# Kernel optimization log

Hardware: AMD Instinct MI355X
Metric: run time of the kernel (lower is better)

## Reference

```python
import jax, jax.numpy as jnp
import numpy as np

D_MODEL = 512
N_HEAD = 8
D_FF = 2048
HEAD = D_MODEL // N_HEAD
B, S = 2, 4096
LN_EPS = 1e-5


def _layernorm(x, g, b):
    mu = jnp.mean(x, axis=-1, keepdims=True)
    var = jnp.mean(jnp.square(x - mu), axis=-1, keepdims=True)
    return (x - mu) * jax.lax.rsqrt(var + LN_EPS) * g + b


def setup_inputs() -> dict:
    key = jax.random.key(0)
    ks = jax.random.split(key, 12)
    s = 0.02
    inp = {
        "src": jax.random.normal(ks[0], (B, S, D_MODEL), dtype=jnp.float32),
        "mask": jnp.ones((B, S, S), dtype=jnp.float32),
        "Wq": jax.random.normal(ks[1], (D_MODEL, D_MODEL), dtype=jnp.float32) * s,
        "bq": jnp.zeros((D_MODEL,), dtype=jnp.float32),
        "Wk": jax.random.normal(ks[2], (D_MODEL, D_MODEL), dtype=jnp.float32) * s,
        "bk": jnp.zeros((D_MODEL,), dtype=jnp.float32),
        "Wv": jax.random.normal(ks[3], (D_MODEL, D_MODEL), dtype=jnp.float32) * s,
        "bv": jnp.zeros((D_MODEL,), dtype=jnp.float32),
        "Wo": jax.random.normal(ks[4], (D_MODEL, D_MODEL), dtype=jnp.float32) * s,
        "bo": jnp.zeros((D_MODEL,), dtype=jnp.float32),
        "W1": jax.random.normal(ks[5], (D_FF, D_MODEL), dtype=jnp.float32) * s,
        "b1": jnp.zeros((D_FF,), dtype=jnp.float32),
        "W2": jax.random.normal(ks[6], (D_MODEL, D_FF), dtype=jnp.float32) * s,
        "b2": jnp.zeros((D_MODEL,), dtype=jnp.float32),
        "ln1_g": jnp.ones((D_MODEL,), dtype=jnp.float32),
        "ln1_b": jnp.zeros((D_MODEL,), dtype=jnp.float32),
        "ln2_g": jnp.ones((D_MODEL,), dtype=jnp.float32),
        "ln2_b": jnp.zeros((D_MODEL,), dtype=jnp.float32),
    }
    return inp


def reference(src, mask, Wq, bq, Wk, bk, Wv, bv, Wo, bo, W1, b1, W2, b2,
              ln1_g, ln1_b, ln2_g, ln2_b):
    # --- multi-head self-attention (chunk/cat == head split on last dim) ---
    def heads(x, W, b):
        y = x @ W.T + b  # [B,S,D]
        return y.reshape(B, S, N_HEAD, HEAD)
    Q = heads(src, Wq, bq)
    K = heads(src, Wk, bk)
    V = heads(src, Wv, bv)
    score = jnp.einsum('bihd,bjhd->bhij', Q, K) / jnp.sqrt(jnp.float32(HEAD))
    score = score + ((1.0 - mask) * -1e9)[:, None, :, :]
    attn = jax.nn.softmax(score, axis=-1)
    ctx = jnp.einsum('bhij,bjhd->bihd', attn, V).reshape(B, S, D_MODEL)
    sa = ctx @ Wo.T + bo
    # --- residual + LN1 ---
    x = _layernorm(src + sa, ln1_g, ln1_b)
    # --- FFN (relu) + residual + LN2 ---
    ff = jax.nn.relu(x @ W1.T + b1) @ W2.T + b2
    return _layernorm(x + ff, ln2_g, ln2_b)
```

## Files before the change

### kernel.cpp

```cpp
#include <hip/hip_runtime.h>
#include <cstdint>
#include <cstddef>

#define DM   512
#define SQL  4096
#define NHE  8
#define HDM  64
#define DFF  2048
#define NB   2

typedef unsigned short u16t;
typedef __attribute__((ext_vector_type(8))) __bf16 bf16x8;
typedef __attribute__((ext_vector_type(4))) float f32x4;
typedef __attribute__((ext_vector_type(8))) unsigned short us8;
typedef __attribute__((ext_vector_type(4))) unsigned short us4;
typedef __attribute__((ext_vector_type(4))) short s16x4;

__device__ inline f32x4 mfma16(bf16x8 a, bf16x8 b, f32x4 c) {
    return __builtin_amdgcn_mfma_f32_16x16x32_bf16(a, b, c, 0, 0, 0);
}
__device__ inline f32x4 mfma16k16(s16x4 a, s16x4 b, f32x4 c) {
    return __builtin_amdgcn_mfma_f32_16x16x16bf16_1k(a, b, c, 0, 0, 0);
}

__device__ inline void load_lds16(const void* g, void* l) {
    __builtin_amdgcn_global_load_lds(
        (const __attribute__((address_space(1))) unsigned int*)g,
        (__attribute__((address_space(3))) unsigned int*)l, 16, 0, 0);
}

__device__ inline u16t f2bf(float x) {
    union { float f; unsigned int u; } v; v.f = x;
    unsigned int r = v.u + 0x7fffu + ((v.u >> 16) & 1u);
    return (u16t)(r >> 16);
}

__device__ inline void store_out(float* C, size_t idx, float v) { C[idx] = v; }
__device__ inline void store_out(u16t* C, size_t idx, float v) { C[idx] = f2bf(v); }

__global__ __launch_bounds__(256) void convert_all(
    const float* __restrict__ src, const float* __restrict__ Wq,
    const float* __restrict__ Wk, const float* __restrict__ Wv,
    const float* __restrict__ Wo, const float* __restrict__ W1,
    const float* __restrict__ W2, const float* __restrict__ bq,
    const float* __restrict__ bk, const float* __restrict__ bv,
    u16t* __restrict__ srcbf, u16t* __restrict__ wqkv, u16t* __restrict__ woc,
    u16t* __restrict__ w1c, u16t* __restrict__ w2c,
    float* __restrict__ bqkv, int* __restrict__ flag) {
    const int blk = blockIdx.x;
    const float* s;
    u16t* d;
    int base;
    if (blk < 2048)      { s = src; d = srcbf;           base = blk; }
    else if (blk < 2176) { s = Wq;  d = wqkv;            base = blk - 2048; }
    else if (blk < 2304) { s = Wk;  d = wqkv + 262144;   base = blk - 2176; }
    else if (blk < 2432) { s = Wv;  d = wqkv + 524288;   base = blk - 2304; }
    else if (blk < 2560) { s = Wo;  d = woc;             base = blk - 2432; }
    else if (blk < 3072) { s = W1;  d = w1c;             base = blk - 2560; }
    else if (blk < 3584) { s = W2;  d = w2c;             base = blk - 3072; }
    else {
        for (int i = threadIdx.x; i < 1536; i += 256)
            bqkv[i] = (i < 512) ? bq[i] : (i < 1024 ? bk[i - 512] : bv[i - 1024]);
        if (threadIdx.x == 0) flag[0] = 1;
        return;
    }
    const int i = base * 2048 + threadIdx.x * 8;
    f32x4 a = *(const f32x4*)(s + i);
    f32x4 b = *(const f32x4*)(s + i + 4);
    us8 o;
    o[0] = f2bf(a[0]); o[1] = f2bf(a[1]); o[2] = f2bf(a[2]); o[3] = f2bf(a[3]);
    o[4] = f2bf(b[0]); o[5] = f2bf(b[1]); o[6] = f2bf(b[2]); o[7] = f2bf(b[3]);
    *(us8*)(d + i) = o;
}

__global__ __launch_bounds__(256) void check_mask_k(const f32x4* __restrict__ m, int* flag) {
    const size_t n4 = (size_t)NB * SQL * SQL / 4;
    size_t i = (size_t)blockIdx.x * 256 + threadIdx.x;
    bool bad = false;
    for (; i < n4; i += (size_t)gridDim.x * 256) {
        f32x4 v = m[i];
        bad |= (v[0] != 1.0f) || (v[1] != 1.0f) || (v[2] != 1.0f) || (v[3] != 1.0f);
    }
    if (bad) flag[0] = 0;
}

template <typename OutT, bool RELU>
__global__ __launch_bounds__(256, 3) void gemm_bt(const u16t* __restrict__ A,
                                                  const u16t* __restrict__ Bw,
                                                  const float* __restrict__ bias,
                                                  OutT* __restrict__ C,
                                                  const int M, const int N, const int K,
                                                  const int ldc) {
    __shared__ u16t As[128 * 32];
    __shared__ u16t Bs[128 * 32];
    const int tid = threadIdx.x;
    const int w = tid >> 6, lane = tid & 63;
    const int l15 = lane & 15, quad = lane >> 4;
    const int m0 = blockIdx.y * 128, n0 = blockIdx.x * 128;
    const int wm = w >> 1, wn = w & 1;

    f32x4 acc[4][4] = {};

    const u16t* Ag = A + ((size_t)(m0 + w * 32 + (lane >> 2))) * K + (lane & 3) * 8;
    const u16t* Bg = Bw + ((size_t)(n0 + w * 32 + (lane >> 2))) * K + (lane & 3) * 8;
    u16t* Asw = &As[(w * 32) * 32];
    u16t* Bsw = &Bs[(w * 32) * 32];

    for (int k0 = 0; k0 < K; k0 += 32) {
        __syncthreads();
        load_lds16(Ag + k0, Asw);
        load_lds16(Ag + (size_t)16 * K + k0, Asw + 16 * 32);
        load_lds16(Bg + k0, Bsw);
        load_lds16(Bg + (size_t)16 * K + k0, Bsw + 16 * 32);
        __syncthreads();
        bf16x8 af[4], bfr[4];
#pragma unroll
        for (int mt = 0; mt < 4; ++mt)
            af[mt] = *(const bf16x8*)&As[(wm * 64 + mt * 16 + l15) * 32 + quad * 8];
#pragma unroll
        for (int nt = 0; nt < 4; ++nt)
            bfr[nt] = *(const bf16x8*)&Bs[(wn * 64 + nt * 16 + l15) * 32 + quad * 8];
#pragma unroll
        for (int mt = 0; mt < 4; ++mt)
#pragma unroll
            for (int nt = 0; nt < 4; ++nt)
                acc[mt][nt] = mfma16(af[mt], bfr[nt], acc[mt][nt]);
    }

    float bv[4];
#pragma unroll
    for (int nt = 0; nt < 4; ++nt) bv[nt] = bias[n0 + wn * 64 + nt * 16 + l15];
#pragma unroll
    for (int mt = 0; mt < 4; ++mt)
#pragma unroll
        for (int r = 0; r < 4; ++r) {
            const int row = m0 + wm * 64 + mt * 16 + quad * 4 + r;
#pragma unroll
            for (int nt = 0; nt < 4; ++nt) {
                float v = acc[mt][nt][r] + bv[nt];
                if (RELU) v = fmaxf(v, 0.0f);
                store_out(C, (size_t)row * ldc + n0 + wn * 64 + nt * 16 + l15, v);
            }
        }
}

__global__ __launch_bounds__(256) void transpose_v(const u16t* __restrict__ qkv,
                                                   u16t* __restrict__ vt) {
    __shared__ u16t t[64 * 72];
    const int sb = blockIdx.x, h = blockIdx.y, b = blockIdx.z;
    const int tid = threadIdx.x;
#pragma unroll
    for (int it = 0; it < 2; ++it) {
        const int idx = it * 256 + tid;
        const int r = idx >> 3, c8 = idx & 7;
        const u16t* gp = qkv + (size_t)(b * SQL + sb * 64 + r) * (3 * DM) + 2 * DM + h * HDM + c8 * 8;
        *(us8*)&t[r * 72 + c8 * 8] = *(const us8*)gp;
    }
    __syncthreads();
#pragma unroll
    for (int it = 0; it < 2; ++it) {
        const int idx = it * 256 + tid;
        const int d = idx >> 3, s8 = idx & 7;
        us8 o;
#pragma unroll
        for (int u = 0; u < 8; ++u) o[u] = t[(s8 * 8 + u) * 72 + d];
        u16t* gp = vt + (size_t)((b * NHE + h) * HDM + d) * SQL + sb * 64 + s8 * 8;
        *(us8*)gp = o;
    }
}

__global__ __launch_bounds__(256, 2) void flash_attn(const u16t* __restrict__ qkv,
                                                     const u16t* __restrict__ vtg,
                                                     const float* __restrict__ mask,
                                                     const int* __restrict__ flag,
                                                     u16t* __restrict__ ctx) {
    __shared__ u16t Ks[128 * 64];
    __shared__ u16t Vs[64 * 128];

    const int qt = blockIdx.x, h = blockIdx.y, b = blockIdx.z;
    const int tid = threadIdx.x;
    const int w = tid >> 6, lane = tid & 63;
    const int l15 = lane & 15, quad = lane >> 4;
    const int e3 = l15 & 7;
    const bool allones = (*flag != 0);

    bf16x8 qf[2][2];
#pragma unroll
    for (int mt = 0; mt < 2; ++mt) {
        const size_t rowb = (size_t)(b * SQL + qt * 128 + w * 32 + mt * 16 + l15) * (3 * DM) + h * HDM;
#pragma unroll
        for (int kk = 0; kk < 2; ++kk)
            qf[mt][kk] = *(const bf16x8*)(qkv + rowb + kk * 32 + quad * 8);
    }

    f32x4 oacc[4][2] = {};
    float m_r[2] = {-3.0e38f, -3.0e38f};
    float l_r[2] = {0.0f, 0.0f};

    const int r8 = lane >> 3, c8 = lane & 7;
    const int r4 = lane >> 4, c16 = lane & 15;

    for (int kt = 0; kt < SQL / 128; ++kt) {
        const int j0 = kt * 128;
        __syncthreads();
#pragma unroll
        for (int i = 0; i < 4; ++i) {
            const int row = j0 + w * 32 + i * 8 + r8;
            load_lds16(qkv + (size_t)(b * SQL + row) * (3 * DM) + DM + h * HDM + ((c8 ^ r8) * 8),
                       &Ks[(w * 32 + i * 8) * 64]);
        }
#pragma unroll
        for (int i = 0; i < 4; ++i) {
            const int d = w * 16 + i * 4 + r4;
            load_lds16(vtg + (size_t)((b * NHE + h) * HDM + d) * SQL + j0 + ((c16 ^ ((i * 4 + r4) & 7)) * 8),
                       &Vs[(w * 16 + i * 4) * 128]);
        }
        __syncthreads();

        f32x4 sacc[2][8] = {};
#pragma unroll
        for (int kk = 0; kk < 2; ++kk) {
#pragma unroll
            for (int jt = 0; jt < 8; ++jt) {
                bf16x8 af = *(const bf16x8*)&Ks[(jt * 16 + l15) * 64 + (((kk * 4 + quad) ^ e3) * 8)];
                sacc[0][jt] = mfma16(af, qf[0][kk], sacc[0][jt]);
                sacc[1][jt] = mfma16(af, qf[1][kk], sacc[1][jt]);
            }
        }

        float av[2][4];
#pragma unroll
        for (int mt = 0; mt < 2; ++mt) {
            if (!allones) {
                const int gi = qt * 128 + w * 32 + mt * 16 + l15;
#pragma unroll
                for (int jt = 0; jt < 8; ++jt)
#pragma unroll
                    for (int r = 0; r < 4; ++r) {
                        const int gj = j0 + jt * 16 + quad * 4 + r;
                        sacc[mt][jt][r] = sacc[mt][jt][r] * 0.125f
                                        + (1.0f - mask[((size_t)b * SQL + gi) * SQL + gj]) * (-1.0e9f);
                    }
            }
            float mx = -3.0e38f;
#pragma unroll
            for (int jt = 0; jt < 8; ++jt)
#pragma unroll
                for (int r = 0; r < 4; ++r) mx = fmaxf(mx, sacc[mt][jt][r]);
            mx = fmaxf(mx, __shfl_xor(mx, 16));
            mx = fmaxf(mx, __shfl_xor(mx, 32));
            const float cs = allones ? 0.18033688011112042f : 1.4426950408889634f;
            const float mnew = fmaxf(m_r[mt], mx);
            const float mb = mnew * cs;
            const float alpha = exp2f(fmaf(m_r[mt], cs, -mb));
            m_r[mt] = mnew;
            float rsum = 0.0f;
#pragma unroll
            for (int jt = 0; jt < 8; ++jt)
#pragma unroll
                for (int r = 0; r < 4; ++r) {
                    const float p = exp2f(fmaf(sacc[mt][jt][r], cs, -mb));
                    sacc[mt][jt][r] = p;
                    rsum += p;
                }
            rsum += __shfl_xor(rsum, 16);
            rsum += __shfl_xor(rsum, 32);
            l_r[mt] = l_r[mt] * alpha + rsum;
#pragma unroll
            for (int r = 0; r < 4; ++r) av[mt][r] = __shfl(alpha, quad * 4 + r);
#pragma unroll
            for (int dt = 0; dt < 4; ++dt)
#pragma unroll
                for (int r = 0; r < 4; ++r) oacc[dt][mt][r] *= av[mt][r];
        }

#pragma unroll
        for (int jt = 0; jt < 8; ++jt) {
            s16x4 pa0, pa1;
#pragma unroll
            for (int r = 0; r < 4; ++r) {
                pa0[r] = (short)f2bf(sacc[0][jt][r]);
                pa1[r] = (short)f2bf(sacc[1][jt][r]);
            }
            const int vcol = (((2 * jt + (quad >> 1)) ^ e3) * 8) + (quad & 1) * 4;
#pragma unroll
            for (int dt = 0; dt < 4; ++dt) {
                s16x4 vb = *(const s16x4*)&Vs[(dt * 16 + l15) * 128 + vcol];
                oacc[dt][0] = mfma16k16(pa0, vb, oacc[dt][0]);
                oacc[dt][1] = mfma16k16(pa1, vb, oacc[dt][1]);
            }
        }
    }

#pragma unroll
    for (int mt = 0; mt < 2; ++mt) {
        float lv[4];
#pragma unroll
        for (int r = 0; r < 4; ++r) lv[r] = __shfl(l_r[mt], quad * 4 + r);
#pragma unroll
        for (int r = 0; r < 4; ++r) {
            const float inv = 1.0f / lv[r];
            const int token = qt * 128 + w * 32 + mt * 16 + quad * 4 + r;
            const size_t base = (size_t)(b * SQL + token) * DM + h * HDM;
#pragma unroll
            for (int dt = 0; dt < 4; ++dt)
                ctx[base + dt * 16 + l15] = f2bf(oacc[dt][mt][r] * inv);
        }
    }
}

template <bool WBF>
__global__ __launch_bounds__(256) void ln_fused(const float* __restrict__ xa,
                                                const float* __restrict__ xb,
                                                const float* __restrict__ g,
                                                const float* __restrict__ be,
                                                float* __restrict__ outf,
                                                u16t* __restrict__ outh) {
    const int row = blockIdx.x * 4 + (threadIdx.x >> 6);
    const int lane = threadIdx.x & 63;
    const size_t base = (size_t)row * DM;
    f32x4 a0 = *(const f32x4*)(xa + base + lane * 4);
    f32x4 b0 = *(const f32x4*)(xb + base + lane * 4);
    f32x4 a1 = *(const f32x4*)(xa + base + 256 + lane * 4);
    f32x4 b1 = *(const f32x4*)(xb + base + 256 + lane * 4);
    f32x4 v0 = a0 + b0, v1 = a1 + b1;
    float s = v0[0] + v0[1] + v0[2] + v0[3] + v1[0] + v1[1] + v1[2] + v1[3];
    float q = v0[0]*v0[0] + v0[1]*v0[1] + v0[2]*v0[2] + v0[3]*v0[3]
            + v1[0]*v1[0] + v1[1]*v1[1] + v1[2]*v1[2] + v1[3]*v1[3];
#pragma unroll
    for (int off = 1; off < 64; off <<= 1) {
        s += __shfl_xor(s, off);
        q += __shfl_xor(q, off);
    }
    const float mean = s * (1.0f / DM);
    const float var = q * (1.0f / DM) - mean * mean;
    const float rs = rsqrtf(var + 1e-5f);
    f32x4 g0 = *(const f32x4*)(g + lane * 4);
    f32x4 g1 = *(const f32x4*)(g + 256 + lane * 4);
    f32x4 e0 = *(const f32x4*)(be + lane * 4);
    f32x4 e1 = *(const f32x4*)(be + 256 + lane * 4);
    f32x4 y0, y1;
#pragma unroll
    for (int i = 0; i < 4; ++i) {
        y0[i] = (v0[i] - mean) * rs * g0[i] + e0[i];
        y1[i] = (v1[i] - mean) * rs * g1[i] + e1[i];
    }
    *(f32x4*)(outf + base + lane * 4) = y0;
    *(f32x4*)(outf + base + 256 + lane * 4) = y1;
    if (WBF) {
        us4 h0, h1;
#pragma unroll
        for (int i = 0; i < 4; ++i) { h0[i] = f2bf(y0[i]); h1[i] = f2bf(y1[i]); }
        *(us4*)(outh + base + lane * 4) = h0;
        *(us4*)(outh + base + 256 + lane * 4) = h1;
    }
}

extern "C" void kernel_launch(void* const* d_in, const int* in_sizes, int n_in,
                              void* d_out, int out_size, void* d_ws, size_t ws_size,
                              hipStream_t stream) {
    const float* src  = (const float*)d_in[0];
    const float* mask = (const float*)d_in[1];
    const float* Wq = (const float*)d_in[2];
    const float* bq = (const float*)d_in[3];
    const float* Wk = (const float*)d_in[4];
    const float* bk = (const float*)d_in[5];
    const float* Wv = (const float*)d_in[6];
    const float* bv = (const float*)d_in[7];
    const float* Wo = (const float*)d_in[8];
    const float* bo = (const float*)d_in[9];
    const float* W1 = (const float*)d_in[10];
    const float* b1 = (const float*)d_in[11];
    const float* W2 = (const float*)d_in[12];
    const float* b2 = (const float*)d_in[13];
    const float* ln1g = (const float*)d_in[14];
    const float* ln1b = (const float*)d_in[15];
    const float* ln2g = (const float*)d_in[16];
    const float* ln2b = (const float*)d_in[17];

    const int M = NB * SQL;

    char* p = (char*)d_ws;
    auto take = [&](size_t bytes) {
        char* r = p;
        p += (bytes + 1023) & ~(size_t)1023;
        return r;
    };
    u16t* regA   = (u16t*)take((size_t)M * DFF * 2);
    u16t* vtb    = (u16t*)take((size_t)NB * NHE * HDM * SQL * 2);
    u16t* ctxb   = (u16t*)take((size_t)M * DM * 2);
    float* sa_ff = (float*)take((size_t)M * DM * 4);
    float* x1f   = (float*)take((size_t)M * DM * 4);
    u16t* x1h    = (u16t*)take((size_t)M * DM * 2);
    u16t* srcbf  = (u16t*)take((size_t)M * DM * 2);
    u16t* wqkv   = (u16t*)take((size_t)3 * DM * DM * 2);
    float* bqkv  = (float*)take((size_t)3 * DM * 4);
    u16t* woc    = (u16t*)take((size_t)DM * DM * 2);
    u16t* w1c    = (u16t*)take((size_t)DFF * DM * 2);
    u16t* w2c    = (u16t*)take((size_t)DM * DFF * 2);
    int* flag    = (int*)take(1024);
    u16t* qkvb   = regA;
    u16t* hbuf   = regA;

    convert_all<<<3585, 256, 0, stream>>>(src, Wq, Wk, Wv, Wo, W1, W2, bq, bk, bv,
                                          srcbf, wqkv, woc, w1c, w2c, bqkv, flag);
    check_mask_k<<<4096, 256, 0, stream>>>((const f32x4*)mask, flag);

    gemm_bt<u16t, false><<<dim3(12, 64), 256, 0, stream>>>(srcbf, wqkv, bqkv, qkvb,
                                                           M, 3 * DM, DM, 3 * DM);
    transpose_v<<<dim3(SQL / 64, NHE, NB), 256, 0, stream>>>(qkvb, vtb);
    flash_attn<<<dim3(SQL / 128, NHE, NB), 256, 0, stream>>>(qkvb, vtb, mask, flag, ctxb);
    gemm_bt<float, false><<<dim3(4, 64), 256, 0, stream>>>(ctxb, woc, bo, sa_ff,
                                                           M, DM, DM, DM);
    ln_fused<true><<<M / 4, 256, 0, stream>>>(src, sa_ff, ln1g, ln1b, x1f, x1h);
    gemm_bt<u16t, true><<<dim3(16, 64), 256, 0, stream>>>(x1h, w1c, b1, hbuf,
                                                          M, DFF, DM, DFF);
    gemm_bt<float, false><<<dim3(4, 64), 256, 0, stream>>>(hbuf, w2c, b2, sa_ff,
                                                           M, DM, DFF, DM);
    ln_fused<false><<<M / 4, 256, 0, stream>>>(x1f, sa_ff, ln2g, ln2b, (float*)d_out,
                                               (u16t*)nullptr);
}
```

Before: 518.1 us.

## Fold mask check into convert kernel, add native exp2, packed bf16, narrower GEMM tiles

Moves the all-ones mask scan into the conversion kernel as extra blocks, which removes one launch. The flag now defaults to not-bad and is set to a sentinel when a non-one entry is found. Flash attention switches to the native exp2 intrinsic and packs probability pairs into bf16 with a perm instruction that rounds half-up instead of to nearest-even. The GEMM gets a templated N tile, and the two N=512 GEMMs use 64-wide tiles so they launch twice as many blocks and fill more CUs.

```diff
diff --git a/kernel.cpp b/kernel.cpp
--- a/kernel.cpp
+++ b/kernel.cpp
@@ -16,6 +16,9 @@
 typedef __attribute__((ext_vector_type(4))) unsigned short us4;
 typedef __attribute__((ext_vector_type(4))) short s16x4;
 
+extern "C" __device__ float __ocml_native_exp2_f32(float);
+__device__ inline float ex2(float x) { return __ocml_native_exp2_f32(x); }
+
 __device__ inline f32x4 mfma16(bf16x8 a, bf16x8 b, f32x4 c) {
     return __builtin_amdgcn_mfma_f32_16x16x32_bf16(a, b, c, 0, 0, 0);
 }
@@ -33,6 +36,12 @@
     union { float f; unsigned int u; } v; v.f = x;
     unsigned int r = v.u + 0x7fffu + ((v.u >> 16) & 1u);
     return (u16t)(r >> 16);
+}
+
+__device__ inline unsigned int pk_bf2(float lo, float hi) {
+    union { float f; unsigned int u; } a, b;
+    a.f = lo; b.f = hi;
+    return __builtin_amdgcn_perm(b.u + 0x8000u, a.u + 0x8000u, 0x07060302u);
 }
 
 __device__ inline void store_out(float* C, size_t idx, float v) { C[idx] = v; }
@@ -44,6 +53,7 @@
     const float* __restrict__ Wo, const float* __restrict__ W1,
     const float* __restrict__ W2, const float* __restrict__ bq,
     const float* __restrict__ bk, const float* __restrict__ bv,
+    const f32x4* __restrict__ mask4,
     u16t* __restrict__ srcbf, u16t* __restrict__ wqkv, u16t* __restrict__ woc,
     u16t* __restrict__ w1c, u16t* __restrict__ w2c,
     float* __restrict__ bqkv, int* __restrict__ flag) {
@@ -58,10 +68,19 @@
     else if (blk < 2560) { s = Wo;  d = woc;             base = blk - 2432; }
     else if (blk < 3072) { s = W1;  d = w1c;             base = blk - 2560; }
     else if (blk < 3584) { s = W2;  d = w2c;             base = blk - 3072; }
-    else {
+    else if (blk == 3584) {
         for (int i = threadIdx.x; i < 1536; i += 256)
             bqkv[i] = (i < 512) ? bq[i] : (i < 1024 ? bk[i - 512] : bv[i - 1024]);
-        if (threadIdx.x == 0) flag[0] = 1;
+        return;
+    } else {
+        const size_t n4 = (size_t)NB * SQL * SQL / 4;
+        size_t i = (size_t)(blk - 3585) * 256 + threadIdx.x;
+        bool bad = false;
+        for (; i < n4; i += (size_t)2048 * 256) {
+            f32x4 v = mask4[i];
+            bad |= (v[0] != 1.0f) || (v[1] != 1.0f) || (v[2] != 1.0f) || (v[3] != 1.0f);
+        }
+        if (bad) flag[0] = 42;
         return;
     }
     const int i = base * 2048 + threadIdx.x * 8;
@@ -73,18 +92,7 @@
     *(us8*)(d + i) = o;
 }
 
-__global__ __launch_bounds__(256) void check_mask_k(const f32x4* __restrict__ m, int* flag) {
-    const size_t n4 = (size_t)NB * SQL * SQL / 4;
-    size_t i = (size_t)blockIdx.x * 256 + threadIdx.x;
-    bool bad = false;
-    for (; i < n4; i += (size_t)gridDim.x * 256) {
-        f32x4 v = m[i];
-        bad |= (v[0] != 1.0f) || (v[1] != 1.0f) || (v[2] != 1.0f) || (v[3] != 1.0f);
-    }
-    if (bad) flag[0] = 0;
-}
-
-template <typename OutT, bool RELU>
+template <typename OutT, bool RELU, int BN>
 __global__ __launch_bounds__(256, 3) void gemm_bt(const u16t* __restrict__ A,
                                                   const u16t* __restrict__ Bw,
                                                   const float* __restrict__ bias,
@@ -92,54 +100,56 @@
                                                   const int M, const int N, const int K,
                                                   const int ldc) {
     __shared__ u16t As[128 * 32];
-    __shared__ u16t Bs[128 * 32];
+    __shared__ u16t Bs[BN * 32];
+    constexpr int NT = BN / 32;
     const int tid = threadIdx.x;
     const int w = tid >> 6, lane = tid & 63;
     const int l15 = lane & 15, quad = lane >> 4;
-    const int m0 = blockIdx.y * 128, n0 = blockIdx.x * 128;
+    const int m0 = blockIdx.y * 128, n0 = blockIdx.x * BN;
     const int wm = w >> 1, wn = w & 1;
 
-    f32x4 acc[4][4] = {};
+    f32x4 acc[4][NT] = {};
 
     const u16t* Ag = A + ((size_t)(m0 + w * 32 + (lane >> 2))) * K + (lane & 3) * 8;
-    const u16t* Bg = Bw + ((size_t)(n0 + w * 32 + (lane >> 2))) * K + (lane & 3) * 8;
+    const u16t* Bg = Bw + ((size_t)(n0 + w * (BN / 4) + (lane >> 2))) * K + (lane & 3) * 8;
     u16t* Asw = &As[(w * 32) * 32];
-    u16t* Bsw = &Bs[(w * 32) * 32];
+    u16t* Bsw = &Bs[(w * (BN / 4)) * 32];
 
     for (int k0 = 0; k0 < K; k0 += 32) {
         __syncthreads();
         load_lds16(Ag + k0, Asw);
         load_lds16(Ag + (size_t)16 * K + k0, Asw + 16 * 32);
-        load_lds16(Bg + k0, Bsw);
-        load_lds16(Bg + (size_t)16 * K + k0, Bsw + 16 * 32);
+#pragma unroll
+        for (int i = 0; i < BN / 64; ++i)
+            load_lds16(Bg + (size_t)(16 * i) * K + k0, Bsw + i * 16 * 32);
         __syncthreads();
-        bf16x8 af[4], bfr[4];
+        bf16x8 af[4], bfr[NT];
 #pragma unroll
         for (int mt = 0; mt < 4; ++mt)
             af[mt] = *(const bf16x8*)&As[(wm * 64 + mt * 16 + l15) * 32 + quad * 8];
 #pragma unroll
-        for (int nt = 0; nt < 4; ++nt)
-            bfr[nt] = *(const bf16x8*)&Bs[(wn * 64 + nt * 16 + l15) * 32 + quad * 8];
+        for (int nt = 0; nt < NT; ++nt)
+            bfr[nt] = *(const bf16x8*)&Bs[(wn * (BN / 2) + nt * 16 + l15) * 32 + quad * 8];
 #pragma unroll
         for (int mt = 0; mt < 4; ++mt)
 #pragma unroll
-            for (int nt = 0; nt < 4; ++nt)
+            for (int nt = 0; nt < NT; ++nt)
                 acc[mt][nt] = mfma16(af[mt], bfr[nt], acc[mt][nt]);
     }
 
-    float bv[4];
-#pragma unroll
-    for (int nt = 0; nt < 4; ++nt) bv[nt] = bias[n0 + wn * 64 + nt * 16 + l15];
+    float bv[NT];
+#pragma unroll
+    for (int nt = 0; nt < NT; ++nt) bv[nt] = bias[n0 + wn * (BN / 2) + nt * 16 + l15];
 #pragma unroll
     for (int mt = 0; mt < 4; ++mt)
 #pragma unroll
         for (int r = 0; r < 4; ++r) {
             const int row = m0 + wm * 64 + mt * 16 + quad * 4 + r;
 #pragma unroll
-            for (int nt = 0; nt < 4; ++nt) {
+            for (int nt = 0; nt < NT; ++nt) {
                 float v = acc[mt][nt][r] + bv[nt];
                 if (RELU) v = fmaxf(v, 0.0f);
-                store_out(C, (size_t)row * ldc + n0 + wn * 64 + nt * 16 + l15, v);
+                store_out(C, (size_t)row * ldc + n0 + wn * (BN / 2) + nt * 16 + l15, v);
             }
         }
 }
@@ -182,7 +192,7 @@
     const int w = tid >> 6, lane = tid & 63;
     const int l15 = lane & 15, quad = lane >> 4;
     const int e3 = l15 & 7;
-    const bool allones = (*flag != 0);
+    const bool allones = (*flag != 42);
 
     bf16x8 qf[2][2];
 #pragma unroll
@@ -252,14 +262,14 @@
             const float cs = allones ? 0.18033688011112042f : 1.4426950408889634f;
             const float mnew = fmaxf(m_r[mt], mx);
             const float mb = mnew * cs;
-            const float alpha = exp2f(fmaf(m_r[mt], cs, -mb));
+            const float alpha = ex2(fmaf(m_r[mt], cs, -mb));
             m_r[mt] = mnew;
             float rsum = 0.0f;
 #pragma unroll
             for (int jt = 0; jt < 8; ++jt)
 #pragma unroll
                 for (int r = 0; r < 4; ++r) {
-                    const float p = exp2f(fmaf(sacc[mt][jt][r], cs, -mb));
+                    const float p = ex2(fmaf(sacc[mt][jt][r], cs, -mb));
                     sacc[mt][jt][r] = p;
                     rsum += p;
                 }
@@ -276,18 +286,17 @@
 
 #pragma unroll
         for (int jt = 0; jt < 8; ++jt) {
-            s16x4 pa0, pa1;
-#pragma unroll
-            for (int r = 0; r < 4; ++r) {
-                pa0[r] = (short)f2bf(sacc[0][jt][r]);
-                pa1[r] = (short)f2bf(sacc[1][jt][r]);
-            }
+            union { s16x4 v; unsigned int u[2]; } pa0, pa1;
+            pa0.u[0] = pk_bf2(sacc[0][jt][0], sacc[0][jt][1]);
+            pa0.u[1] = pk_bf2(sacc[0][jt][2], sacc[0][jt][3]);
+            pa1.u[0] = pk_bf2(sacc[1][jt][0], sacc[1][jt][1]);
+            pa1.u[1] = pk_bf2(sacc[1][jt][2], sacc[1][jt][3]);
             const int vcol = (((2 * jt + (quad >> 1)) ^ e3) * 8) + (quad & 1) * 4;
 #pragma unroll
             for (int dt = 0; dt < 4; ++dt) {
                 s16x4 vb = *(const s16x4*)&Vs[(dt * 16 + l15) * 128 + vcol];
-                oacc[dt][0] = mfma16k16(pa0, vb, oacc[dt][0]);
-                oacc[dt][1] = mfma16k16(pa1, vb, oacc[dt][1]);
+                oacc[dt][0] = mfma16k16(pa0.v, vb, oacc[dt][0]);
+                oacc[dt][1] = mfma16k16(pa1.v, vb, oacc[dt][1]);
             }
         }
     }
@@ -402,21 +411,21 @@
     u16t* qkvb   = regA;
     u16t* hbuf   = regA;
 
-    convert_all<<<3585, 256, 0, stream>>>(src, Wq, Wk, Wv, Wo, W1, W2, bq, bk, bv,
+    convert_all<<<5633, 256, 0, stream>>>(src, Wq, Wk, Wv, Wo, W1, W2, bq, bk, bv,
+                                          (const f32x4*)mask,
                                           srcbf, wqkv, woc, w1c, w2c, bqkv, flag);
-    check_mask_k<<<4096, 256, 0, stream>>>((const f32x4*)mask, flag);
-
-    gemm_bt<u16t, false><<<dim3(12, 64), 256, 0, stream>>>(srcbf, wqkv, bqkv, qkvb,
-                                                           M, 3 * DM, DM, 3 * DM);
+
+    gemm_bt<u16t, false, 128><<<dim3(12, 64), 256, 0, stream>>>(srcbf, wqkv, bqkv, qkvb,
+                                                                M, 3 * DM, DM, 3 * DM);
     transpose_v<<<dim3(SQL / 64, NHE, NB), 256, 0, stream>>>(qkvb, vtb);
     flash_attn<<<dim3(SQL / 128, NHE, NB), 256, 0, stream>>>(qkvb, vtb, mask, flag, ctxb);
-    gemm_bt<float, false><<<dim3(4, 64), 256, 0, stream>>>(ctxb, woc, bo, sa_ff,
-                                                           M, DM, DM, DM);
+    gemm_bt<float, false, 64><<<dim3(8, 64), 256, 0, stream>>>(ctxb, woc, bo, sa_ff,
+                                                               M, DM, DM, DM);
     ln_fused<true><<<M / 4, 256, 0, stream>>>(src, sa_ff, ln1g, ln1b, x1f, x1h);
-    gemm_bt<u16t, true><<<dim3(16, 64), 256, 0, stream>>>(x1h, w1c, b1, hbuf,
-                                                          M, DFF, DM, DFF);
-    gemm_bt<float, false><<<dim3(4, 64), 256, 0, stream>>>(hbuf, w2c, b2, sa_ff,
-                                                           M, DM, DFF, DM);
+    gemm_bt<u16t, true, 128><<<dim3(16, 64), 256, 0, stream>>>(x1h, w1c, b1, hbuf,
+                                                               M, DFF, DM, DFF);
+    gemm_bt<float, false, 64><<<dim3(8, 64), 256, 0, stream>>>(hbuf, w2c, b2, sa_ff,
+                                                               M, DM, DFF, DM);
     ln_fused<false><<<M / 4, 256, 0, stream>>>(x1f, sa_ff, ln2g, ln2b, (float*)d_out,
                                                (u16t*)nullptr);
 }
```

Measured after the change: 471.4 us. -9.0%, faster.
